# Kernel optimization log

Measured on AMD Instinct MI355X. Metric: run time of the kernel, lower is better.

The kernel has to match this reference:

```python
import jax, jax.numpy as jnp
import numpy as np

ALPHA = 10.0
BETA = 0.05
FAR_DELTA = 1e10  # matches torch 10000000000.0 padding for the last delta


def sdf_to_density(signed_distance, alpha, beta):
    s = -signed_distance
    return jnp.where(
        s <= 0,
        alpha * (0.5 * jnp.exp(s / beta)),
        alpha * (1.0 - 0.5 * jnp.exp(-s / beta)),
    )


def setup_inputs() -> dict:
    key = jax.random.key(0)
    k1, k2, k3 = jax.random.split(key, 3)
    R, N = 65536, 128
    distance = jax.random.normal(k1, (R, N), dtype=jnp.float32)  # SDF values
    color = jax.random.uniform(k2, (R, N, 3), dtype=jnp.float32)
    # per-ray sorted sample depths in [2, 6] (near/far)
    t = jax.random.uniform(k3, (R, N), dtype=jnp.float32)
    depth_values = jnp.sort(2.0 + 4.0 * t, axis=-1)
    return {"distance": distance, "color": color, "depth_values": depth_values}


def reference(distance, color, depth_values):
    # deltas: [R, N], last delta padded with a huge value
    deltas = jnp.concatenate(
        [depth_values[:, 1:] - depth_values[:, :-1],
         jnp.full_like(depth_values[:, :1], FAR_DELTA)],
        axis=-1,
    )
    density = sdf_to_density(distance, ALPHA, BETA)  # [R, N]
    d = density * deltas  # [R, N]
    # transmittance: exp(-cumsum of previous densities), exclusive scan
    trans = jnp.exp(-jnp.concatenate(
        [jnp.zeros_like(d[:, :1]), jnp.cumsum(d[:, :-1], axis=-1)], axis=-1))
    weights = (1.0 - jnp.exp(-d)) * trans  # [R, N]
    out_color = jnp.sum(weights[..., None] * color, axis=-2)  # [R, 3]
    geometry = jnp.zeros_like(color)  # faithful to geometry_color = zeros_like(color)
    return out_color, geometry
```

## Files before the change

kernel.cpp:

```cpp
#include <hip/hip_runtime.h>

#define ALPHA     10.0f
#define INV_BETA  20.0f
#define FAR_DELTA 1e10f
#define NSAMP     128

__device__ __forceinline__ float laplace_density(float sdf) {
    float s = -sdf;
    float e = __expf(-fabsf(s) * INV_BETA);
    return (s <= 0.f) ? (0.5f * ALPHA * e) : (ALPHA * (1.f - 0.5f * e));
}

__global__ __launch_bounds__(256) void volsdf_render(
    const float* __restrict__ dist,
    const float* __restrict__ color,
    const float* __restrict__ depth,
    float*       __restrict__ out,
    int R)
{
    const int lane   = threadIdx.x & 63;
    const int waveId = threadIdx.x >> 6;
    const int sub    = lane & 31;
    const int half   = lane >> 5;
    const int rayPair = blockIdx.x * 4 + waveId;
    const int ray     = rayPair * 2 + half;
    if (ray >= R) return;

    const size_t rbase = (size_t)ray * NSAMP;

    float4 di = ((const float4*)(dist  + rbase))[sub];
    float4 dp = ((const float4*)(depth + rbase))[sub];
    const float* cp = color + rbase * 3 + (size_t)sub * 12;
    float4 c0 = ((const float4*)cp)[0];
    float4 c1 = ((const float4*)cp)[1];
    float4 c2 = ((const float4*)cp)[2];

    float* geo = out + (size_t)R * 3 + (size_t)rayPair * 768;
    float4 z4 = make_float4(0.f, 0.f, 0.f, 0.f);
    ((float4*)geo)[lane]       = z4;
    ((float4*)geo)[64  + lane] = z4;
    ((float4*)geo)[128 + lane] = z4;

    float nx  = __shfl_down(dp.x, 1, 32);
    float dl0 = dp.y - dp.x;
    float dl1 = dp.z - dp.y;
    float dl2 = dp.w - dp.z;
    float dl3 = (sub == 31) ? FAR_DELTA : (nx - dp.w);

    float d0 = laplace_density(di.x) * dl0;
    float d1 = laplace_density(di.y) * dl1;
    float d2 = laplace_density(di.z) * dl2;
    float d3 = laplace_density(di.w) * dl3;

    float local = (d0 + d1) + (d2 + d3);
    float incl  = local;
    #pragma unroll
    for (int off = 1; off < 32; off <<= 1) {
        float v = __shfl_up(incl, off, 32);
        if (sub >= off) incl += v;
    }
    float base = __shfl_up(incl, 1, 32);
    if (sub == 0) base = 0.f;

    float p1 = base + d0, p2 = p1 + d1, p3 = p2 + d2;
    float w0 = (1.f - __expf(-d0)) * __expf(-base);
    float w1 = (1.f - __expf(-d1)) * __expf(-p1);
    float w2 = (1.f - __expf(-d2)) * __expf(-p2);
    float w3 = (1.f - __expf(-d3)) * __expf(-p3);

    float ar = (w0 * c0.x + w1 * c0.w) + (w2 * c1.z + w3 * c2.y);
    float ag = (w0 * c0.y + w1 * c1.x) + (w2 * c1.w + w3 * c2.z);
    float ab = (w0 * c0.z + w1 * c1.y) + (w2 * c2.x + w3 * c2.w);

    #pragma unroll
    for (int off = 16; off > 0; off >>= 1) {
        ar += __shfl_down(ar, off, 32);
        ag += __shfl_down(ag, off, 32);
        ab += __shfl_down(ab, off, 32);
    }
    if (sub == 0) {
        out[(size_t)ray * 3 + 0] = ar;
        out[(size_t)ray * 3 + 1] = ag;
        out[(size_t)ray * 3 + 2] = ab;
    }
}

extern "C" void kernel_launch(void* const* d_in, const int* in_sizes, int n_in,
                              void* d_out, int out_size, void* d_ws, size_t ws_size,
                              hipStream_t stream) {
    const float* dist  = (const float*)d_in[0];
    const float* color = (const float*)d_in[1];
    const float* depth = (const float*)d_in[2];
    float* out = (float*)d_out;

    const int R = in_sizes[0] / NSAMP;
    const int blocks = (R + 7) / 8;

    hipLaunchKernelGGL(volsdf_render, dim3(blocks), dim3(256), 0, stream,
                       dist, color, depth, out, R);
}
```

Measured before the change: 224.2 us.

## Use persistent grid-stride waves with double-buffered register prefetch of ray pairs

Replaces the one-ray-pair-per-wave launch with a fixed grid of 1024 blocks whose waves loop over ray pairs in a grid-stride pattern. Each wave loads the next pair's distance, depth and color into a second register set while it processes the current pair, to hide global memory latency. This raises register pressure and lowers the number of waves in flight compared with the original large grid. It also drops handling of an odd ray count, since nPairs = R>>1.

```diff
diff --git a/kernel.cpp b/kernel.cpp
--- a/kernel.cpp
+++ b/kernel.cpp
@@ -16,72 +16,100 @@
     const float* __restrict__ color,
     const float* __restrict__ depth,
     float*       __restrict__ out,
-    int R)
+    int R, int nWaves)
 {
-    const int lane   = threadIdx.x & 63;
-    const int waveId = threadIdx.x >> 6;
-    const int sub    = lane & 31;
-    const int half   = lane >> 5;
-    const int rayPair = blockIdx.x * 4 + waveId;
-    const int ray     = rayPair * 2 + half;
-    if (ray >= R) return;
+    const int lane = threadIdx.x & 63;
+    const int sub  = lane & 31;
+    const int half = lane >> 5;
+    const int gw   = blockIdx.x * 4 + (threadIdx.x >> 6);
+    const int nPairs = R >> 1;
 
-    const size_t rbase = (size_t)ray * NSAMP;
+    float* geoBase = out + (size_t)R * 3;
 
-    float4 di = ((const float4*)(dist  + rbase))[sub];
-    float4 dp = ((const float4*)(depth + rbase))[sub];
-    const float* cp = color + rbase * 3 + (size_t)sub * 12;
-    float4 c0 = ((const float4*)cp)[0];
-    float4 c1 = ((const float4*)cp)[1];
-    float4 c2 = ((const float4*)cp)[2];
+    auto loadPair = [&](int rp, float4& di, float4& dp,
+                        float4& c0, float4& c1, float4& c2) {
+        const size_t rbase = (size_t)(rp * 2 + half) * NSAMP;
+        di = ((const float4*)(dist  + rbase))[sub];
+        dp = ((const float4*)(depth + rbase))[sub];
+        const float* cp = color + rbase * 3 + (size_t)sub * 12;
+        c0 = ((const float4*)cp)[0];
+        c1 = ((const float4*)cp)[1];
+        c2 = ((const float4*)cp)[2];
+    };
 
-    float* geo = out + (size_t)R * 3 + (size_t)rayPair * 768;
-    float4 z4 = make_float4(0.f, 0.f, 0.f, 0.f);
-    ((float4*)geo)[lane]       = z4;
-    ((float4*)geo)[64  + lane] = z4;
-    ((float4*)geo)[128 + lane] = z4;
+    auto process = [&](int rp, float4 di, float4 dp,
+                       float4 c0, float4 c1, float4 c2) {
+        float4* geo = (float4*)(geoBase + (size_t)rp * 768);
+        float4 z4 = make_float4(0.f, 0.f, 0.f, 0.f);
+        geo[lane]       = z4;
+        geo[64  + lane] = z4;
+        geo[128 + lane] = z4;
 
-    float nx  = __shfl_down(dp.x, 1, 32);
-    float dl0 = dp.y - dp.x;
-    float dl1 = dp.z - dp.y;
-    float dl2 = dp.w - dp.z;
-    float dl3 = (sub == 31) ? FAR_DELTA : (nx - dp.w);
+        float nx  = __shfl_down(dp.x, 1, 32);
+        float dl0 = dp.y - dp.x;
+        float dl1 = dp.z - dp.y;
+        float dl2 = dp.w - dp.z;
+        float dl3 = (sub == 31) ? FAR_DELTA : (nx - dp.w);
 
-    float d0 = laplace_density(di.x) * dl0;
-    float d1 = laplace_density(di.y) * dl1;
-    float d2 = laplace_density(di.z) * dl2;
-    float d3 = laplace_density(di.w) * dl3;
+        float d0 = laplace_density(di.x) * dl0;
+        float d1 = laplace_density(di.y) * dl1;
+        float d2 = laplace_density(di.z) * dl2;
+        float d3 = laplace_density(di.w) * dl3;
 
-    float local = (d0 + d1) + (d2 + d3);
-    float incl  = local;
-    #pragma unroll
-    for (int off = 1; off < 32; off <<= 1) {
-        float v = __shfl_up(incl, off, 32);
-        if (sub >= off) incl += v;
-    }
-    float base = __shfl_up(incl, 1, 32);
-    if (sub == 0) base = 0.f;
+        float local = (d0 + d1) + (d2 + d3);
+        float incl  = local;
+        #pragma unroll
+        for (int off = 1; off < 32; off <<= 1) {
+            float v = __shfl_up(incl, off, 32);
+            if (sub >= off) incl += v;
+        }
+        float base = __shfl_up(incl, 1, 32);
+        if (sub == 0) base = 0.f;
 
-    float p1 = base + d0, p2 = p1 + d1, p3 = p2 + d2;
-    float w0 = (1.f - __expf(-d0)) * __expf(-base);
-    float w1 = (1.f - __expf(-d1)) * __expf(-p1);
-    float w2 = (1.f - __expf(-d2)) * __expf(-p2);
-    float w3 = (1.f - __expf(-d3)) * __expf(-p3);
+        float p1 = base + d0, p2 = p1 + d1, p3 = p2 + d2;
+        float w0 = (1.f - __expf(-d0)) * __expf(-base);
+        float w1 = (1.f - __expf(-d1)) * __expf(-p1);
+        float w2 = (1.f - __expf(-d2)) * __expf(-p2);
+        float w3 = (1.f - __expf(-d3)) * __expf(-p3);
 
-    float ar = (w0 * c0.x + w1 * c0.w) + (w2 * c1.z + w3 * c2.y);
-    float ag = (w0 * c0.y + w1 * c1.x) + (w2 * c1.w + w3 * c2.z);
-    float ab = (w0 * c0.z + w1 * c1.y) + (w2 * c2.x + w3 * c2.w);
+        float ar = (w0 * c0.x + w1 * c0.w) + (w2 * c1.z + w3 * c2.y);
+        float ag = (w0 * c0.y + w1 * c1.x) + (w2 * c1.w + w3 * c2.z);
+        float ab = (w0 * c0.z + w1 * c1.y) + (w2 * c2.x + w3 * c2.w);
 
-    #pragma unroll
-    for (int off = 16; off > 0; off >>= 1) {
-        ar += __shfl_down(ar, off, 32);
-        ag += __shfl_down(ag, off, 32);
-        ab += __shfl_down(ab, off, 32);
-    }
-    if (sub == 0) {
-        out[(size_t)ray * 3 + 0] = ar;
-        out[(size_t)ray * 3 + 1] = ag;
-        out[(size_t)ray * 3 + 2] = ab;
+        #pragma unroll
+        for (int off = 16; off > 0; off >>= 1) {
+            ar += __shfl_down(ar, off, 32);
+            ag += __shfl_down(ag, off, 32);
+            ab += __shfl_down(ab, off, 32);
+        }
+        if (sub == 0) {
+            int ray = rp * 2 + half;
+            out[(size_t)ray * 3 + 0] = ar;
+            out[(size_t)ray * 3 + 1] = ag;
+            out[(size_t)ray * 3 + 2] = ab;
+        }
+    };
+
+    float4 diA, dpA, c0A, c1A, c2A;
+    float4 diB, dpB, c0B, c1B, c2B;
+
+    int rp0 = gw;
+    if (rp0 >= nPairs) return;
+    loadPair(rp0, diA, dpA, c0A, c1A, c2A);
+
+    while (true) {
+        int rp1 = rp0 + nWaves;
+        bool have1 = rp1 < nPairs;
+        if (have1) loadPair(rp1, diB, dpB, c0B, c1B, c2B);
+        process(rp0, diA, dpA, c0A, c1A, c2A);
+        if (!have1) return;
+
+        int rp2 = rp1 + nWaves;
+        bool have2 = rp2 < nPairs;
+        if (have2) loadPair(rp2, diA, dpA, c0A, c1A, c2A);
+        process(rp1, diB, dpB, c0B, c1B, c2B);
+        if (!have2) return;
+        rp0 = rp2;
     }
 }
 
@@ -94,8 +122,13 @@
     float* out = (float*)d_out;
 
     const int R = in_sizes[0] / NSAMP;
-    const int blocks = (R + 7) / 8;
+    const int nPairs = R >> 1;
+
+    int blocks = 1024;
+    int maxBlocks = (nPairs + 3) / 4;
+    if (blocks > maxBlocks) blocks = maxBlocks;
+    const int nWaves = blocks * 4;
 
     hipLaunchKernelGGL(volsdf_render, dim3(blocks), dim3(256), 0, stream,
-                       dist, color, depth, out, R);
+                       dist, color, depth, out, R, nWaves);
 }
```

New measurement: 227.3 us. No clear change (+1.4%).
